# Kernel tuning notes

Measured on AMD Instinct MI355X. Metric: run time of the kernel, lower is better.

The kernel has to match this reference:

```python
import jax, jax.numpy as jnp
import numpy as np

B, N, F_IN = 32, 512, 64
HEADS = (8, 8)
HIDS = (64, 64)
EDGE_P = 0.05  # graph density
NEG_SLOPE = 0.2
NEG_INF = -1e20


def setup_inputs() -> dict:
    key = jax.random.key(0)
    ks = jax.random.split(key, 8)
    x = jax.random.normal(ks[0], (B, N, F_IN), dtype=jnp.float32)
    adj = (jax.random.uniform(ks[1], (B, N, N)) < EDGE_P).astype(jnp.float32)
    adj = jnp.maximum(adj, adj.transpose(0, 2, 1))  # symmetric adjacency
    # mask = (batch, row): every (b, n) pair gets the masked softmax
    b_idx = jnp.repeat(jnp.arange(B, dtype=jnp.int32), N)   # [B*N]
    r_idx = jnp.tile(jnp.arange(N, dtype=jnp.int32), B)     # [B*N]
    # layer 0: f_in=64 -> f_out=64, H=8 ; layer 1: f_in=64*8=512 -> f_out=64, H=8
    W0 = jax.random.normal(ks[2], (F_IN, HIDS[0]), dtype=jnp.float32) / jnp.sqrt(jnp.float32(F_IN))
    a_src0 = jax.random.normal(ks[3], (HIDS[0], HEADS[0]), dtype=jnp.float32) / jnp.sqrt(jnp.float32(HIDS[0]))
    a_dst0 = jax.random.normal(ks[4], (HIDS[0], HEADS[0]), dtype=jnp.float32) / jnp.sqrt(jnp.float32(HIDS[0]))
    f_in1 = HIDS[0] * HEADS[0]
    W1 = jax.random.normal(ks[5], (f_in1, HIDS[1]), dtype=jnp.float32) / jnp.sqrt(jnp.float32(f_in1))
    a_src1 = jax.random.normal(ks[6], (HIDS[1], HEADS[1]), dtype=jnp.float32) / jnp.sqrt(jnp.float32(HIDS[1]))
    a_dst1 = jax.random.normal(ks[7], (HIDS[1], HEADS[1]), dtype=jnp.float32) / jnp.sqrt(jnp.float32(HIDS[1]))
    return dict(x=x, adj=adj, b_idx=b_idx, r_idx=r_idx,
                W0=W0, a_src0=a_src0, a_dst0=a_dst0,
                W1=W1, a_src1=a_src1, a_dst1=a_dst1)


def _gat_layer(x, adj, b_idx, r_idx, W, a_src, a_dst):
    # x: [B,N,f_in], adj: [B,N,N] (diag already set), W: [f_in,F], a_*: [F,H]
    hp = x @ W                                        # [B,N,F]
    s = jnp.einsum('bnf,fh->bhn', hp, a_src)          # attn_src
    d = jnp.einsum('bnf,fh->bhn', hp, a_dst)          # attn_dst
    attn = s[:, :, :, None] + d[:, :, None, :]        # [B,H,N,N]
    attn = jnp.where(attn >= 0, attn, NEG_SLOPE * attn)  # leaky_relu(0.2)
    attn = jnp.where(adj[:, None, :, :] == 0, 0.0, attn)  # masked_fill(adj==0, 0)
    rows = attn[b_idx, :, r_idx, :]                   # [K,H,N]
    rows = jnp.where(rows == 0.0, NEG_INF, rows)
    rows = jax.nn.softmax(rows, axis=-1)
    attn = attn.at[b_idx, :, r_idx, :].set(rows)
    return jnp.einsum('bhij,bjf->bhif', attn, hp)     # [B,H,N,F]


def reference(x, adj, b_idx, r_idx, W0, a_src0, a_dst0, W1, a_src1, a_dst1):
    Bn, Nn = x.shape[:2]
    # torch mutates adj in place: adj[batch,row,row] = 1 (self loops)
    adj = adj.at[b_idx, r_idx, r_idx].set(1.0)
    o = _gat_layer(x, adj, b_idx, r_idx, W0, a_src0, a_dst0)      # [B,H,N,F0]
    x1 = jax.nn.elu(o.transpose(0, 2, 1, 3).reshape(Bn, Nn, -1))  # [B,N,H*F0]
    o2 = _gat_layer(x1, adj, b_idx, r_idx, W1, a_src1, a_dst1)    # [B,H,N,F1]
    return o2.mean(axis=1)                                        # [B,N,F1]
```

## Files before the change

### kernel.cpp

```cpp
#include <hip/hip_runtime.h>
#include <hip/hip_bf16.h>
#include <math.h>

#define BB 32
#define NN 512

typedef _Float16 f16x8 __attribute__((ext_vector_type(8)));
typedef __fp16  fp16x2 __attribute__((ext_vector_type(2)));
typedef float f32x4 __attribute__((ext_vector_type(4)));

#define MFMA16(a, b, c) __builtin_amdgcn_mfma_f32_16x16x32_f16(a, b, c, 0, 0, 0)

union AF { f16x8 v; unsigned int u[4]; };

__device__ __forceinline__ void gload_lds16(const void* g, void* l) {
    __builtin_amdgcn_global_load_lds(
        (const __attribute__((address_space(1))) unsigned int*)g,
        (__attribute__((address_space(3))) unsigned int*)l, 16, 0, 0);
}
__device__ __forceinline__ void gload_lds4(const void* g, void* l) {
    __builtin_amdgcn_global_load_lds(
        (const __attribute__((address_space(1))) unsigned int*)g,
        (__attribute__((address_space(3))) unsigned int*)l, 4, 0, 0);
}

__device__ __forceinline__ unsigned fenc(float f) {
    unsigned b = __float_as_uint(f);
    return (b & 0x80000000u) ? ~b : (b | 0x80000000u);
}
__device__ __forceinline__ float fdec(unsigned u) {
    return __uint_as_float((u & 0x80000000u) ? (u ^ 0x80000000u) : ~u);
}

__global__ __launch_bounds__(256) void k_wt_prep(
    const float* __restrict__ W0, _Float16* __restrict__ W0T,
    const float* __restrict__ W1, _Float16* __restrict__ W1T,
    unsigned* __restrict__ maxdz)
{
    int id = blockIdx.x * 256 + threadIdx.x;
    if (id < 512) maxdz[id] = 0u;
    const float* W; _Float16* WT; int KT, task;
    if (id < 512) { W = W0; WT = W0T; KT = 64;  task = id; }
    else          { W = W1; WT = W1T; KT = 512; task = id - 512; }
    int n = task & 63, gabs = task >> 6;
    int c = gabs >> 3, g = gabs & 7;
    f16x8 hv;
#pragma unroll
    for (int e = 0; e < 8; ++e)
        hv[e] = (_Float16)W[(size_t)(gabs * 8 + e) * 64 + n];
    *(f16x8*)(WT + (size_t)n * KT + c * 64 + (g ^ (n & 7)) * 8) = hv;
}

static __device__ __forceinline__ void epi16(
    const float* ctile, const float* asd_f, int row0, int t,
    float* __restrict__ s, float* __restrict__ dTg, _Float16* __restrict__ hpT,
    float* dmax_lds, unsigned* __restrict__ maxd_out)
{
    int b = row0 >> 9, jb = row0 & 511;
    if (t < 128) {
        int rr = t >> 3, h = t & 7;
        float sv = 0.f, dv = 0.f;
#pragma unroll
        for (int f = 0; f < 64; ++f) {
            float hv = ctile[rr * 66 + f];
            sv = fmaf(hv, asd_f[f * 8 + h], sv);
            dv = fmaf(hv, asd_f[512 + f * 8 + h], dv);
        }
        s[((size_t)b * NN + jb + rr) * 8 + h] = sv;
        dTg[((size_t)b * 8 + h) * NN + jb + rr] = dv;
        dmax_lds[t] = dv;
    } else if (t < 256) {
        int t2 = t - 128;
        int f = t2 >> 1, jl = (t2 & 1) * 8;
        f16x8 hv;
#pragma unroll
        for (int e = 0; e < 8; ++e)
            hv[e] = (_Float16)ctile[(jl + e) * 66 + f];
        *(f16x8*)(hpT + ((size_t)b * 64 + f) * NN + jb + jl) = hv;
    }
    __syncthreads();
    if (t < 8) {
        float m = dmax_lds[t];
#pragma unroll
        for (int k = 1; k < 16; ++k) m = fmaxf(m, dmax_lds[t + 8 * k]);
        atomicMax(maxd_out + (b * 8 + t), fenc(m));
    }
}

static __device__ __forceinline__ void epi32(
    const float* ctile, const float* asd_f, int row0, int t,
    float* __restrict__ s, float* __restrict__ dTg, _Float16* __restrict__ hpT,
    float* dmax_lds, unsigned* __restrict__ maxd_out)
{
    int b = row0 >> 9, jb = row0 & 511;
    if (t < 256) {
        int rr = t >> 3, h = t & 7;
        float sv = 0.f, dv = 0.f;
#pragma unroll
        for (int f = 0; f < 64; ++f) {
            float hv = ctile[rr * 66 + f];
            sv = fmaf(hv, asd_f[f * 8 + h], sv);
            dv = fmaf(hv, asd_f[512 + f * 8 + h], dv);
        }
        s[((size_t)b * NN + jb + rr) * 8 + h] = sv;
        dTg[((size_t)b * 8 + h) * NN + jb + rr] = dv;
        dmax_lds[t] = dv;
    } else {
        int t2 = t - 256;
        int f = t2 >> 2, jl = (t2 & 3) * 8;
        f16x8 hv;
#pragma unroll
        for (int e = 0; e < 8; ++e)
            hv[e] = (_Float16)ctile[(jl + e) * 66 + f];
        *(f16x8*)(hpT + ((size_t)b * 64 + f) * NN + jb + jl) = hv;
    }
    __syncthreads();
    if (t < 8) {
        float m = dmax_lds[t];
#pragma unroll
        for (int k = 1; k < 32; ++k) m = fmaxf(m, dmax_lds[t + 8 * k]);
        atomicMax(maxd_out + (b * 8 + t), fenc(m));
    }
}

__global__ __launch_bounds__(256) void k_gemm0(
    const float* __restrict__ x, const _Float16* __restrict__ W0T,
    const float* __restrict__ a_src, const float* __restrict__ a_dst,
    const float* __restrict__ adj, unsigned long long* __restrict__ adjb,
    float* __restrict__ s, float* __restrict__ dTg, _Float16* __restrict__ hpT,
    unsigned* __restrict__ maxd)
{
    __shared__ float ctile[16 * 66];
    __shared__ float asd_f[1024];
    __shared__ unsigned int mrow[16][16];
    __shared__ float dmax[128];
    int t = threadIdx.x, row0 = blockIdx.x * 16;
    int lane = t & 63, w = t >> 6, cn = lane & 15, rq = lane >> 4;

    int ar = t >> 4, seg = t & 15;
    const float* ap = adj + (size_t)(row0 + ar) * NN + seg * 32;
    float4 av[8];
#pragma unroll
    for (int q = 0; q < 8; ++q) av[q] = ((const float4*)ap)[q];

    ((float4*)asd_f)[t] = (t < 128) ? ((const float4*)a_src)[t]
                                    : ((const float4*)a_dst)[t - 128];
    f32x4 acc;
#pragma unroll
    for (int e = 0; e < 4; ++e) acc[e] = 0.f;
#pragma unroll
    for (int ks = 0; ks < 2; ++ks) {
        const float* xp = x + (size_t)(row0 + cn) * 64 + ks * 32 + rq * 8;
        float4 x0 = *(const float4*)xp, x1 = *(const float4*)(xp + 4);
        f16x8 ah = {(_Float16)x0.x, (_Float16)x0.y, (_Float16)x0.z, (_Float16)x0.w,
                    (_Float16)x1.x, (_Float16)x1.y, (_Float16)x1.z, (_Float16)x1.w};
        int nn = w * 16 + cn;
        f16x8 bh = *(const f16x8*)(W0T + (size_t)nn * 64 + (((ks * 4 + rq) ^ (nn & 7)) * 8));
        acc = MFMA16(ah, bh, acc);
    }
#pragma unroll
    for (int r = 0; r < 4; ++r)
        ctile[(rq * 4 + r) * 66 + w * 16 + cn] = acc[r];
    __syncthreads();
    epi16(ctile, asd_f, row0, t, s, dTg, hpT, dmax, maxd);

    unsigned int m32 = 0;
#pragma unroll
    for (int q = 0; q < 8; ++q) {
        if (av[q].x != 0.f) m32 |= 1u << (q * 4 + 0);
        if (av[q].y != 0.f) m32 |= 1u << (q * 4 + 1);
        if (av[q].z != 0.f) m32 |= 1u << (q * 4 + 2);
        if (av[q].w != 0.f) m32 |= 1u << (q * 4 + 3);
    }
    int i = (row0 + ar) & (NN - 1);
    if ((i >> 5) == seg) m32 |= 1u << (i & 31);
    mrow[ar][seg] = m32;
    __syncthreads();
    if (t < 128) {
        int r = t >> 3, k = t & 7;
        unsigned long long u = (unsigned long long)mrow[r][2 * k]
                             | ((unsigned long long)mrow[r][2 * k + 1] << 32);
        adjb[(size_t)(row0 + r) * 8 + k] = u;
    }
}

#define PBUILD(AOUT, SV, M_, MBYTE, DDv)                                \
    do {                                                                \
        _Pragma("unroll")                                               \
        for (int e = 0; e < 8; e += 2) {                                \
            float pA[2];                                                \
            _Pragma("unroll")                                           \
            for (int q = 0; q < 2; ++q) {                               \
                int ee = e + q;                                         \
                bool con = (MBYTE >> ee) & 1u;                          \
                float e0 = SV + DDv[ee];                                \
                float l0 = fmaxf(e0, 0.2f * e0);                        \
                float p0 = __expf(l0 - M_);                             \
                pA[q] = (con && l0 != 0.f) ? p0 : 0.f;                  \
            }                                                           \
            fp16x2 ka = __builtin_amdgcn_cvt_pkrtz(pA[0], pA[1]);       \
            AOUT.u[e >> 1] = __builtin_bit_cast(unsigned int, ka);      \
        }                                                               \
    } while (0)

template<int MODE>
__global__ __launch_bounds__(512, 4) void k_attn_fused(
    const unsigned long long* __restrict__ adjb, const float* __restrict__ s,
    const float* __restrict__ dTg, const unsigned* __restrict__ maxd,
    const _Float16* __restrict__ hpT,
    const _Float16* __restrict__ W1T,
    const float* __restrict__ a_src, const float* __restrict__ a_dst,
    float* __restrict__ s_out, float* __restrict__ dTg_out,
    _Float16* __restrict__ hpT_out, unsigned* __restrict__ maxd_out,
    float* __restrict__ o_f)
{
    __shared__ __align__(16) char smem[38400];
    char* bufP = smem;
    char* bufQ = smem + 10240;

    int blk = blockIdx.x;
    int vb = ((blk & 7) << 6) | (blk >> 3);
    int b = vb >> 4, i0 = (vb & 15) << 5;
    int row0 = vb * 32;
    int t = threadIdx.x, lane = t & 63, w = t >> 6;
    int cn = lane & 15, rq = lane >> 4;
    int myrow = i0 + cn;

    const _Float16* hb = hpT + (size_t)b * 64 * NN;
    int f0 = t >> 3, g0 = t & 7;
    const _Float16* hsrc = hb + (size_t)f0 * NN + ((g0 ^ (f0 & 7)) * 8);
    const float* dsrc = dTg + ((size_t)b * 8 + w) * NN + lane;

    {
        gload_lds16(hsrc, (_Float16*)bufP + (w << 9));
        gload_lds4(dsrc, (float*)(bufP + 8192) + (w << 6));
    }

    float svA = s[((size_t)b * NN + myrow) * 8 + w];
    float svB = s[((size_t)b * NN + myrow + 16) * 8 + w];
    float md = fdec(maxd[b * 8 + w]);
    float MA = fmaxf(svA + md, 0.f);
    float MB = fmaxf(svB + md, 0.f);
    const unsigned long long* abr = adjb + ((size_t)b * NN + myrow) * 8;
    int rq8 = rq * 8;

    f16x8 ones;
#pragma unroll
    for (int e = 0; e < 8; ++e) ones[e] = (_Float16)1.0f;

    f32x4 accA[4], accB[4], accrsA, accrsB;
#pragma unroll
    for (int e = 0; e < 4; ++e) { accrsA[e] = 0.f; accrsB[e] = 0.f; }
#pragma unroll
    for (int ft = 0; ft < 4; ++ft)
#pragma unroll
        for (int e = 0; e < 4; ++e) { accA[ft][e] = 0.f; accB[ft][e] = 0.f; }

    unsigned long long mbA = abr[0], mbB = abr[128];
    __syncthreads();

    for (int jcx = 0; jcx < 8; ++jcx) {
        int jc = jcx * 64;
        char* cur = (jcx & 1) ? bufQ : bufP;
        char* nxt = (jcx & 1) ? bufP : bufQ;
        if (jcx < 7) {
            gload_lds16(hsrc + jc + 64, (_Float16*)nxt + (w << 9));
            gload_lds4(dsrc + jc + 64, (float*)(nxt + 8192) + (w << 6));
        }
        unsigned long long mbnA = (jcx < 7) ? abr[jcx + 1] : 0ull;
        unsigned long long mbnB = (jcx < 7) ? abr[jcx + 129] : 0ull;
        const _Float16* hTc = (const _Float16*)cur;
        const float* ddl = (const float*)(cur + 8192) + (w << 6);
        unsigned int mlA = (unsigned)mbA, mhA = (unsigned)(mbA >> 32);
        unsigned int mlB = (unsigned)mbB, mhB = (unsigned)(mbB >> 32);
#pragma unroll
        for (int ks = 0; ks < 2; ++ks) {
            float dd[8];
            *(float4*)&dd[0] = *(const float4*)(ddl + ks * 32 + rq8);
            *(float4*)&dd[4] = *(const float4*)(ddl + ks * 32 + rq8 + 4);
            unsigned int mbyA = ((ks ? mhA : mlA) >> rq8) & 0xffu;
            unsigned int mbyB = ((ks ? mhB : mlB) >> rq8) & 0xffu;
            AF aA, aB;
            PBUILD(aA, svA, MA, mbyA, dd);
            PBUILD(aB, svB, MB, mbyB, dd);
            accrsA = MFMA16(aA.v, ones, accrsA);
            accrsB = MFMA16(aB.v, ones, accrsB);
#pragma unroll
            for (int ft = 0; ft < 4; ++ft) {
                int f = ft * 16 + cn;
                f16x8 bh = *(const f16x8*)&hTc[f * 64 + (((ks * 4 + rq) ^ (f & 7)) * 8)];
                accA[ft] = MFMA16(aA.v, bh, accA[ft]);
                accB[ft] = MFMA16(aB.v, bh, accB[ft]);
            }
        }
        mbA = mbnA; mbB = mbnB;
        __syncthreads();
    }

    float invrA[4], invrB[4];
#pragma unroll
    for (int r = 0; r < 4; ++r) {
        invrA[r] = 1.0f / accrsA[r];
        invrB[r] = 1.0f / accrsB[r];
    }

    if (MODE == 0) {
        _Float16* x1all = (_Float16*)smem;
#pragma unroll
        for (int rt = 0; rt < 2; ++rt)
#pragma unroll
            for (int ft = 0; ft < 4; ++ft)
#pragma unroll
                for (int r = 0; r < 4; ++r) {
                    int il = rt * 16 + rq * 4 + r;
                    float v = rt ? accB[ft][r] * invrB[r]
                                 : accA[ft][r] * invrA[r];
                    v = v > 0.f ? v : __expf(v) - 1.f;
                    int f = ft * 16 + cn;
                    x1all[w * 2048 + il * 64 + (((f >> 3) ^ (il & 7)) * 8) + (f & 7)] =
                        (_Float16)v;
                }
        __syncthreads();
        f32x4 g1A, g1B;
#pragma unroll
        for (int e = 0; e < 4; ++e) { g1A[e] = 0.f; g1B[e] = 0.f; }
        int nn = (w & 3) * 16 + cn, kh = w >> 2;
        const _Float16* wb = W1T + (size_t)nn * 512;
#pragma unroll
        for (int kc2 = 0; kc2 < 4; ++kc2) {
            int kc = kh * 4 + kc2;
#pragma unroll
            for (int ks = 0; ks < 2; ++ks) {
                f16x8 bh = *(const f16x8*)(wb + kc * 64 +
                                           (((ks * 4 + rq) ^ (nn & 7)) * 8));
                f16x8 ahA = *(const f16x8*)&x1all[kc * 2048 + cn * 64 +
                                                  (((ks * 4 + rq) ^ (cn & 7)) * 8)];
                f16x8 ahB = *(const f16x8*)&x1all[kc * 2048 + (16 + cn) * 64 +
                                                  (((ks * 4 + rq) ^ (cn & 7)) * 8)];
                g1A = MFMA16(ahA, bh, g1A);
                g1B = MFMA16(ahB, bh, g1B);
            }
        }
        __syncthreads();
        float* ct = (float*)smem;
        float* asd_f = (float*)(smem + 33280);
        float* dmax = (float*)(smem + 37376);
#pragma unroll
        for (int r = 0; r < 4; ++r) {
            ct[kh * 2112 + (rq * 4 + r) * 66 + nn] = g1A[r];
            ct[kh * 2112 + (16 + rq * 4 + r) * 66 + nn] = g1B[r];
        }
        if (t < 256)
            ((float4*)asd_f)[t] = (t < 128) ? ((const float4*)a_src)[t]
                                            : ((const float4*)a_dst)[t - 128];
        __syncthreads();
        for (int idx = t; idx < 2112; idx += 512) ct[idx] += ct[2112 + idx];
        __syncthreads();
        epi32(ct, asd_f, row0, t, s_out, dTg_out, hpT_out, dmax, maxd_out);
    } else {
        float* red = (float*)smem;
#pragma unroll
        for (int ph = 0; ph < 2; ++ph) {
            if ((w >> 2) == ph) {
#pragma unroll
                for (int rt = 0; rt < 2; ++rt)
#pragma unroll
                    for (int ft = 0; ft < 4; ++ft)
#pragma unroll
                        for (int r = 0; r < 4; ++r) {
                            int il = rt * 16 + rq * 4 + r;
                            float v = rt ? accB[ft][r] * invrB[r]
                                         : accA[ft][r] * invrA[r];
                            int off = (w & 3) * 2048 + il * 64 + ft * 16 + cn;
                            if (ph == 0) red[off] = v;
                            else         red[off] += v;
                        }
            }
            __syncthreads();
        }
#pragma unroll
        for (int u = 0; u < 4; ++u) {
            int idx = t + u * 512;
            int il = idx >> 6, f = idx & 63;
            float sum = red[il * 64 + f] + red[2048 + il * 64 + f]
                      + red[4096 + il * 64 + f] + red[6144 + il * 64 + f];
            o_f[((size_t)b * NN + i0 + il) * 64 + f] = sum * 0.125f;
        }
    }
}

extern "C" void kernel_launch(void* const* d_in, const int* in_sizes, int n_in,
                              void* d_out, int out_size, void* d_ws, size_t ws_size,
                              hipStream_t stream) {
    const float* x      = (const float*)d_in[0];
    const float* adj    = (const float*)d_in[1];
    const float* W0     = (const float*)d_in[4];
    const float* a_src0 = (const float*)d_in[5];
    const float* a_dst0 = (const float*)d_in[6];
    const float* W1     = (const float*)d_in[7];
    const float* a_src1 = (const float*)d_in[8];
    const float* a_dst1 = (const float*)d_in[9];
    float* out = (float*)d_out;

    float* ws = (float*)d_ws;
    const size_t R = (size_t)BB * NN;
    const size_t BHN = (size_t)BB * 8 * NN;
    float* s0    = ws;
    float* dTg0  = s0 + R * 8;
    float* s1    = dTg0 + BHN;
    float* dTg1  = s1 + R * 8;
    unsigned* maxd0 = (unsigned*)(dTg1 + BHN);
    unsigned* maxd1 = maxd0 + 256;
    _Float16* hp0T = (_Float16*)(maxd1 + 256);
    _Float16* hp1T = hp0T + (size_t)BB * 64 * NN;
    _Float16* W0T  = hp1T + (size_t)BB * 64 * NN;
    _Float16* W1T  = W0T + (size_t)64 * 64;
    unsigned long long* adjb = (unsigned long long*)(W1T + (size_t)64 * 512);

    k_wt_prep<<<18, 256, 0, stream>>>(W0, W0T, W1, W1T, maxd0);
    k_gemm0<<<1024, 256, 0, stream>>>(x, W0T, a_src0, a_dst0, adj, adjb,
                                      s0, dTg0, hp0T, maxd0);
    k_attn_fused<0><<<512, 512, 0, stream>>>(adjb, s0, dTg0, maxd0, hp0T,
                                             W1T, a_src1, a_dst1,
                                             s1, dTg1, hp1T, maxd1, nullptr);
    k_attn_fused<1><<<512, 512, 0, stream>>>(adjb, s1, dTg1, maxd1, hp1T,
                                             nullptr, nullptr, nullptr,
                                             nullptr, nullptr, nullptr, nullptr, out);
}
```

Baseline: 160.7 us.

## Fold weight prep into front kernel and replace atomic max with partial-max buffers

Removes the separate weight-prep launch. W0 is now read and converted inline in the first GEMM, and the W1 transpose is done by the first 16 blocks of the front kernel. The atomicMax on an encoded per-batch column max, which needed a zeroing pass, is replaced by per-tile partial maxima written to a buffer and reduced with warp shuffles in the consumer kernel. This saves one launch and the atomic contention, at the cost of extra scattered W0 loads per block and a small reduction in each attention block.

```diff
diff --git a/kernel.cpp b/kernel.cpp
--- a/kernel.cpp
+++ b/kernel.cpp
@@ -24,37 +24,10 @@
         (__attribute__((address_space(3))) unsigned int*)l, 4, 0, 0);
 }
 
-__device__ __forceinline__ unsigned fenc(float f) {
-    unsigned b = __float_as_uint(f);
-    return (b & 0x80000000u) ? ~b : (b | 0x80000000u);
-}
-__device__ __forceinline__ float fdec(unsigned u) {
-    return __uint_as_float((u & 0x80000000u) ? (u ^ 0x80000000u) : ~u);
-}
-
-__global__ __launch_bounds__(256) void k_wt_prep(
-    const float* __restrict__ W0, _Float16* __restrict__ W0T,
-    const float* __restrict__ W1, _Float16* __restrict__ W1T,
-    unsigned* __restrict__ maxdz)
-{
-    int id = blockIdx.x * 256 + threadIdx.x;
-    if (id < 512) maxdz[id] = 0u;
-    const float* W; _Float16* WT; int KT, task;
-    if (id < 512) { W = W0; WT = W0T; KT = 64;  task = id; }
-    else          { W = W1; WT = W1T; KT = 512; task = id - 512; }
-    int n = task & 63, gabs = task >> 6;
-    int c = gabs >> 3, g = gabs & 7;
-    f16x8 hv;
-#pragma unroll
-    for (int e = 0; e < 8; ++e)
-        hv[e] = (_Float16)W[(size_t)(gabs * 8 + e) * 64 + n];
-    *(f16x8*)(WT + (size_t)n * KT + c * 64 + (g ^ (n & 7)) * 8) = hv;
-}
-
 static __device__ __forceinline__ void epi16(
     const float* ctile, const float* asd_f, int row0, int t,
     float* __restrict__ s, float* __restrict__ dTg, _Float16* __restrict__ hpT,
-    float* dmax_lds, unsigned* __restrict__ maxd_out)
+    float* dmax_lds, float* __restrict__ pmax_out)
 {
     int b = row0 >> 9, jb = row0 & 511;
     if (t < 128) {
@@ -83,14 +56,14 @@
         float m = dmax_lds[t];
 #pragma unroll
         for (int k = 1; k < 16; ++k) m = fmaxf(m, dmax_lds[t + 8 * k]);
-        atomicMax(maxd_out + (b * 8 + t), fenc(m));
+        pmax_out[((size_t)b * 32 + (jb >> 4)) * 8 + t] = m;
     }
 }
 
 static __device__ __forceinline__ void epi32(
     const float* ctile, const float* asd_f, int row0, int t,
     float* __restrict__ s, float* __restrict__ dTg, _Float16* __restrict__ hpT,
-    float* dmax_lds, unsigned* __restrict__ maxd_out)
+    float* dmax_lds, float* __restrict__ pmax_out)
 {
     int b = row0 >> 9, jb = row0 & 511;
     if (t < 256) {
@@ -119,16 +92,17 @@
         float m = dmax_lds[t];
 #pragma unroll
         for (int k = 1; k < 32; ++k) m = fmaxf(m, dmax_lds[t + 8 * k]);
-        atomicMax(maxd_out + (b * 8 + t), fenc(m));
-    }
-}
-
-__global__ __launch_bounds__(256) void k_gemm0(
-    const float* __restrict__ x, const _Float16* __restrict__ W0T,
+        pmax_out[((size_t)b * 16 + (jb >> 5)) * 8 + t] = m;
+    }
+}
+
+__global__ __launch_bounds__(256) void k_front(
+    const float* __restrict__ x, const float* __restrict__ W0,
+    const float* __restrict__ W1, _Float16* __restrict__ W1T,
     const float* __restrict__ a_src, const float* __restrict__ a_dst,
     const float* __restrict__ adj, unsigned long long* __restrict__ adjb,
     float* __restrict__ s, float* __restrict__ dTg, _Float16* __restrict__ hpT,
-    unsigned* __restrict__ maxd)
+    float* __restrict__ pmax)
 {
     __shared__ float ctile[16 * 66];
     __shared__ float asd_f[1024];
@@ -137,6 +111,17 @@
     int t = threadIdx.x, row0 = blockIdx.x * 16;
     int lane = t & 63, w = t >> 6, cn = lane & 15, rq = lane >> 4;
 
+    if (blockIdx.x < 16) {
+        int task = blockIdx.x * 256 + t;
+        int n = task & 63, gabs = task >> 6;
+        int c = gabs >> 3, g = gabs & 7;
+        f16x8 hv;
+#pragma unroll
+        for (int e = 0; e < 8; ++e)
+            hv[e] = (_Float16)W1[(size_t)(gabs * 8 + e) * 64 + n];
+        *(f16x8*)(W1T + (size_t)n * 512 + c * 64 + (g ^ (n & 7)) * 8) = hv;
+    }
+
     int ar = t >> 4, seg = t & 15;
     const float* ap = adj + (size_t)(row0 + ar) * NN + seg * 32;
     float4 av[8];
@@ -148,21 +133,24 @@
     f32x4 acc;
 #pragma unroll
     for (int e = 0; e < 4; ++e) acc[e] = 0.f;
+    int nn0 = w * 16 + cn;
 #pragma unroll
     for (int ks = 0; ks < 2; ++ks) {
         const float* xp = x + (size_t)(row0 + cn) * 64 + ks * 32 + rq * 8;
         float4 x0 = *(const float4*)xp, x1 = *(const float4*)(xp + 4);
         f16x8 ah = {(_Float16)x0.x, (_Float16)x0.y, (_Float16)x0.z, (_Float16)x0.w,
                     (_Float16)x1.x, (_Float16)x1.y, (_Float16)x1.z, (_Float16)x1.w};
-        int nn = w * 16 + cn;
-        f16x8 bh = *(const f16x8*)(W0T + (size_t)nn * 64 + (((ks * 4 + rq) ^ (nn & 7)) * 8));
+        f16x8 bh;
+#pragma unroll
+        for (int e = 0; e < 8; ++e)
+            bh[e] = (_Float16)W0[(size_t)((ks * 4 + rq) * 8 + e) * 64 + nn0];
         acc = MFMA16(ah, bh, acc);
     }
 #pragma unroll
     for (int r = 0; r < 4; ++r)
         ctile[(rq * 4 + r) * 66 + w * 16 + cn] = acc[r];
     __syncthreads();
-    epi16(ctile, asd_f, row0, t, s, dTg, hpT, dmax, maxd);
+    epi16(ctile, asd_f, row0, t, s, dTg, hpT, dmax, pmax);
 
     unsigned int m32 = 0;
 #pragma unroll
@@ -206,12 +194,12 @@
 template<int MODE>
 __global__ __launch_bounds__(512, 4) void k_attn_fused(
     const unsigned long long* __restrict__ adjb, const float* __restrict__ s,
-    const float* __restrict__ dTg, const unsigned* __restrict__ maxd,
+    const float* __restrict__ dTg, const float* __restrict__ pmaxd,
     const _Float16* __restrict__ hpT,
     const _Float16* __restrict__ W1T,
     const float* __restrict__ a_src, const float* __restrict__ a_dst,
     float* __restrict__ s_out, float* __restrict__ dTg_out,
-    _Float16* __restrict__ hpT_out, unsigned* __restrict__ maxd_out,
+    _Float16* __restrict__ hpT_out, float* __restrict__ pmax_out,
     float* __restrict__ o_f)
 {
     __shared__ __align__(16) char smem[38400];
@@ -236,9 +224,13 @@
         gload_lds4(dsrc, (float*)(bufP + 8192) + (w << 6));
     }
 
+    constexpr int NT = (MODE == 0) ? 32 : 16;
+    float md = pmaxd[((size_t)b * NT + (lane & (NT - 1))) * 8 + w];
+#pragma unroll
+    for (int off = NT >> 1; off; off >>= 1) md = fmaxf(md, __shfl_xor(md, off));
+
     float svA = s[((size_t)b * NN + myrow) * 8 + w];
     float svB = s[((size_t)b * NN + myrow + 16) * 8 + w];
-    float md = fdec(maxd[b * 8 + w]);
     float MA = fmaxf(svA + md, 0.f);
     float MB = fmaxf(svB + md, 0.f);
     const unsigned long long* abr = adjb + ((size_t)b * NN + myrow) * 8;
@@ -356,7 +348,7 @@
         __syncthreads();
         for (int idx = t; idx < 2112; idx += 512) ct[idx] += ct[2112 + idx];
         __syncthreads();
-        epi32(ct, asd_f, row0, t, s_out, dTg_out, hpT_out, dmax, maxd_out);
+        epi32(ct, asd_f, row0, t, s_out, dTg_out, hpT_out, dmax, pmax_out);
     } else {
         float* red = (float*)smem;
 #pragma unroll
@@ -409,21 +401,19 @@
     float* dTg0  = s0 + R * 8;
     float* s1    = dTg0 + BHN;
     float* dTg1  = s1 + R * 8;
-    unsigned* maxd0 = (unsigned*)(dTg1 + BHN);
-    unsigned* maxd1 = maxd0 + 256;
-    _Float16* hp0T = (_Float16*)(maxd1 + 256);
+    float* pmax0 = dTg1 + BHN;
+    float* pmax1 = pmax0 + 8192;
+    _Float16* hp0T = (_Float16*)(pmax1 + 4096);
     _Float16* hp1T = hp0T + (size_t)BB * 64 * NN;
-    _Float16* W0T  = hp1T + (size_t)BB * 64 * NN;
-    _Float16* W1T  = W0T + (size_t)64 * 64;
+    _Float16* W1T  = hp1T + (size_t)BB * 64 * NN;
     unsigned long long* adjb = (unsigned long long*)(W1T + (size_t)64 * 512);
 
-    k_wt_prep<<<18, 256, 0, stream>>>(W0, W0T, W1, W1T, maxd0);
-    k_gemm0<<<1024, 256, 0, stream>>>(x, W0T, a_src0, a_dst0, adj, adjb,
-                                      s0, dTg0, hp0T, maxd0);
-    k_attn_fused<0><<<512, 512, 0, stream>>>(adjb, s0, dTg0, maxd0, hp0T,
+    k_front<<<1024, 256, 0, stream>>>(x, W0, W1, W1T, a_src0, a_dst0,
+                                      adj, adjb, s0, dTg0, hp0T, pmax0);
+    k_attn_fused<0><<<512, 512, 0, stream>>>(adjb, s0, dTg0, pmax0, hp0T,
                                              W1T, a_src1, a_dst1,
-                                             s1, dTg1, hp1T, maxd1, nullptr);
-    k_attn_fused<1><<<512, 512, 0, stream>>>(adjb, s1, dTg1, maxd1, hp1T,
+                                             s1, dTg1, hp1T, pmax1, nullptr);
+    k_attn_fused<1><<<512, 512, 0, stream>>>(adjb, s1, dTg1, pmax1, hp1T,
                                              nullptr, nullptr, nullptr,
                                              nullptr, nullptr, nullptr, nullptr, out);
 }
```

Result: no change. 160.8 us (+0.0%).
